# Optimization experiments

Hardware: AMD Instinct MI355X
Metric: run time of the kernel (lower is better)

Reference implementation:

```python
import jax, jax.numpy as jnp
import numpy as np
import math

B, L, D = 4, 4096, 1024
H = 16
DH = D // H  # 64
MAX_SEQ = 8192
NF_MAX = MAX_SEQ // 2 + 1  # 4097
EPS = 1e-6
SQRT2_INV = 1.0 / math.sqrt(2.0)


def _ln(x, scale, bias, eps=1e-5):
    m = jnp.mean(x, axis=-1, keepdims=True)
    v = jnp.mean((x - m) ** 2, axis=-1, keepdims=True)
    return (x - m) * jax.lax.rsqrt(v + eps) * scale + bias


def setup_inputs() -> dict:
    key = jax.random.key(0)
    ks = jax.random.split(key, 16)
    s = 0.02
    inp = {
        'x': jax.random.normal(ks[0], (B, L, D), dtype=jnp.float32),
        'Wq': jax.random.normal(ks[1], (D, D), dtype=jnp.float32) * s,
        'Wv': jax.random.normal(ks[2], (D, D), dtype=jnp.float32) * s,
        'Wo': jax.random.normal(ks[3], (D, D), dtype=jnp.float32) * s,
        # gate MLP: LayerNorm(Dh) -> Linear(Dh,4Dh) -> GELU -> Linear(4Dh, 2*NF_MAX)
        'ln_g_s': jnp.ones((DH,), jnp.float32),
        'ln_g_b': jnp.zeros((DH,), jnp.float32),
        'W1': jax.random.normal(ks[4], (4 * DH, DH), dtype=jnp.float32) * s,
        'b1': jnp.zeros((4 * DH,), jnp.float32),
        'W2': jax.random.normal(ks[5], (2 * NF_MAX, 4 * DH), dtype=jnp.float32) * s,
        'b2': jnp.zeros((2 * NF_MAX,), jnp.float32),
        'modrelu_bias': jnp.zeros((H, NF_MAX), jnp.float32),
        # wavelet gating MLP on head_dim
        'ln_w_s': jnp.ones((DH,), jnp.float32),
        'ln_w_b': jnp.zeros((DH,), jnp.float32),
        'Ww1': jax.random.normal(ks[6], (DH, DH), dtype=jnp.float32) * s,
        'bw1': jnp.zeros((DH,), jnp.float32),
        'Ww2': jax.random.normal(ks[7], (DH, DH), dtype=jnp.float32) * s,
        'bw2': jnp.zeros((DH,), jnp.float32),
    }
    return inp


def _spectre_forward(x, Wq, Wv, Wo, ln_g_s, ln_g_b, W1, b1, W2, b2,
                     modrelu_bias, ln_w_s, ln_w_b, Ww1, bw1, Ww2, bw2):
    b, l, d = x.shape
    n_freq = l // 2 + 1
    # projections -> (B,H,L,Dh)
    q = jnp.einsum('bld,ed->ble', x, Wq).reshape(b, l, H, DH).transpose(0, 2, 1, 3)
    v = jnp.einsum('bld,ed->ble', x, Wv).reshape(b, l, H, DH).transpose(0, 2, 1, 3)
    q_bar = jnp.mean(q, axis=2)  # (B,H,Dh) global query
    # frequency gates from global query
    h = _ln(q_bar, ln_g_s, ln_g_b)
    h = jax.nn.gelu(jnp.einsum('bhd,fd->bhf', h, W1) + b1, approximate=False)
    g = jnp.einsum('bhf,gf->bhg', h, W2) + b2  # (B,H,2*NF_MAX)
    gate = g[..., :n_freq] + 1j * g[..., NF_MAX:NF_MAX + n_freq]  # (B,H,n_freq)
    # spectral mixing along sequence axis
    Vf = jnp.fft.rfft(v, axis=2)  # (B,H,n_freq,Dh) complex
    Vf = Vf * gate[..., None]
    # modReLU nonlinearity on complex spectrum
    mag = jnp.abs(Vf)
    bias = modrelu_bias[None, :, :n_freq, None]
    Vf = Vf * (jax.nn.relu(mag + bias) / (mag + EPS))
    y = jnp.fft.irfft(Vf, n=l, axis=2)  # (B,H,L,Dh)
    # wavelet refinement (eval mode -> never skipped)
    gw = _ln(q_bar, ln_w_s, ln_w_b)
    gw = jax.nn.gelu(jnp.einsum('bhd,ed->bhe', gw, Ww1) + bw1, approximate=False)
    gw = jax.nn.sigmoid(jnp.einsum('bhd,ed->bhe', gw, Ww2) + bw2)  # (B,H,Dh)
    yc = y.transpose(0, 1, 3, 2)  # (B,H,Dh,L)
    low = (yc[..., 0::2] + yc[..., 1::2]) * SQRT2_INV   # Haar analysis LP
    high = (yc[..., 1::2] - yc[..., 0::2]) * SQRT2_INV  # Haar analysis HP
    low = low * gw[..., None]
    high = high * gw[..., None]
    even = (low - high) * SQRT2_INV   # Haar synthesis
    odd = (low + high) * SQRT2_INV
    rec = jnp.stack([even, odd], axis=-1).reshape(b, H, DH, l)  # interleave
    y = y + rec.transpose(0, 1, 3, 2)
    out = jnp.einsum('bld,ed->ble', y.transpose(0, 2, 1, 3).reshape(b, l, d), Wo)
    return out


def reference(x, Wq, Wv, Wo, ln_g_s, ln_g_b, W1, b1, W2, b2,
              modrelu_bias, ln_w_s, ln_w_b, Ww1, bw1, Ww2, bw2):
    return _spectre_forward(x, Wq, Wv, Wo, ln_g_s, ln_g_b, W1, b1, W2, b2,
                            modrelu_bias, ln_w_s, ln_w_b, Ww1, bw1, Ww2, bw2)
```

## Files before the change

### kernel.cpp

```cpp
#include <hip/hip_runtime.h>
#include <math.h>

#define LSEQ 4096
#define DDIM 1024
#define NB 4
#define NH 16
#define DHD 64
#define NFREQ 2049
#define NFMAX 4097

typedef __bf16 bf16_8 __attribute__((ext_vector_type(8)));
typedef float f32x4 __attribute__((ext_vector_type(4)));

__device__ __forceinline__ float gelu_exact(float v) {
    return 0.5f * v * (1.0f + erff(v * 0.70710678118654752440f));
}

__device__ __forceinline__ void gload16(const void* g, void* l) {
    __builtin_amdgcn_global_load_lds((const __attribute__((address_space(1))) char*)g,
                                     (__attribute__((address_space(3))) char*)l, 16, 0, 0);
}

__global__ __launch_bounds__(256) void k_xbar_partial(const float* __restrict__ x, float* __restrict__ xbp,
                                                      __bf16* __restrict__ xbf) {
    int d = blockIdx.x * 256 + threadIdx.x;
    int chunk = blockIdx.y;
    int b = blockIdx.z;
    size_t base = ((size_t)b * LSEQ + (size_t)chunk * 256) * DDIM + d;
    float acc = 0.f;
    for (int l = 0; l < 256; ++l) {
        float v = x[base + (size_t)l * DDIM];
        acc += v;
        xbf[base + (size_t)l * DDIM] = (__bf16)v;
    }
    xbp[(size_t)(b * 16 + chunk) * DDIM + d] = acc;
}

__global__ __launch_bounds__(256) void k_xbar_reduce(const float* __restrict__ xbp, float* __restrict__ xbar) {
    int d = blockIdx.x * 256 + threadIdx.x;
    int b = blockIdx.y;
    float acc = 0.f;
    for (int c = 0; c < 16; ++c) acc += xbp[(size_t)(b * 16 + c) * DDIM + d];
    xbar[b * DDIM + d] = acc * (1.0f / LSEQ);
}

__global__ __launch_bounds__(256) void k_cvt(const float* __restrict__ s, __bf16* __restrict__ d, int n) {
    int i = (blockIdx.x * 256 + threadIdx.x) * 4;
    if (i < n) {
        float4 v = *(const float4*)(s + i);
        d[i] = (__bf16)v.x; d[i + 1] = (__bf16)v.y; d[i + 2] = (__bf16)v.z; d[i + 3] = (__bf16)v.w;
    }
}

__global__ __launch_bounds__(256) void k_qbar(const float* __restrict__ xbar, const float* __restrict__ Wq,
                                              float* __restrict__ qbar) {
    int lane = threadIdx.x & 63;
    int e = blockIdx.x * 4 + (threadIdx.x >> 6);
    const float* wrow = Wq + (size_t)e * DDIM;
    float a0 = 0, a1 = 0, a2 = 0, a3 = 0;
    for (int i = 0; i < 16; ++i) {
        int d = lane + i * 64;
        float w = wrow[d];
        a0 += w * xbar[d];
        a1 += w * xbar[DDIM + d];
        a2 += w * xbar[2 * DDIM + d];
        a3 += w * xbar[3 * DDIM + d];
    }
    for (int off = 32; off > 0; off >>= 1) {
        a0 += __shfl_down(a0, off);
        a1 += __shfl_down(a1, off);
        a2 += __shfl_down(a2, off);
        a3 += __shfl_down(a3, off);
    }
    if (lane == 0) {
        qbar[e] = a0;
        qbar[DDIM + e] = a1;
        qbar[2 * DDIM + e] = a2;
        qbar[3 * DDIM + e] = a3;
    }
}

__global__ __launch_bounds__(256) void k_mlp(const float* __restrict__ qbar,
                                             const float* __restrict__ ln_g_s, const float* __restrict__ ln_g_b,
                                             const float* __restrict__ W1, const float* __restrict__ b1,
                                             const float* __restrict__ ln_w_s, const float* __restrict__ ln_w_b,
                                             const float* __restrict__ Ww1, const float* __restrict__ bw1,
                                             const float* __restrict__ Ww2, const float* __restrict__ bw2,
                                             float* __restrict__ h1g, float* __restrict__ gwp1) {
    int bh = blockIdx.x;
    __shared__ float q[64], hg[64], hw[64], g1[64];
    __shared__ float sm, sv;
    int t = threadIdx.x;
    if (t < 64) q[t] = qbar[bh * 64 + t];
    __syncthreads();
    if (t == 0) {
        float m = 0;
        for (int i = 0; i < 64; ++i) m += q[i];
        m *= (1.0f / 64.0f);
        float v = 0;
        for (int i = 0; i < 64; ++i) { float dd = q[i] - m; v += dd * dd; }
        v *= (1.0f / 64.0f);
        sm = m; sv = v;
    }
    __syncthreads();
    if (t < 64) {
        float n = (q[t] - sm) * rsqrtf(sv + 1e-5f);
        hg[t] = n * ln_g_s[t] + ln_g_b[t];
        hw[t] = n * ln_w_s[t] + ln_w_b[t];
    }
    __syncthreads();
    {
        int f = t;
        const float* w = W1 + (size_t)f * 64;
        float s = b1[f];
        for (int d0 = 0; d0 < 64; ++d0) s += hg[d0] * w[d0];
        h1g[(size_t)bh * 256 + f] = gelu_exact(s);
    }
    if (t < 64) {
        const float* w = Ww1 + (size_t)t * 64;
        float s = bw1[t];
        for (int k = 0; k < 64; ++k) s += hw[k] * w[k];
        g1[t] = gelu_exact(s);
    }
    __syncthreads();
    if (t < 64) {
        const float* w = Ww2 + (size_t)t * 64;
        float s = bw2[t];
        for (int k = 0; k < 64; ++k) s += g1[k] * w[k];
        gwp1[bh * 64 + t] = 1.0f + 1.0f / (1.0f + expf(-s));
    }
}

__global__ __launch_bounds__(256) void k_gate(const float* __restrict__ h1g, const float* __restrict__ W2,
                                              const float* __restrict__ b2,
                                              float* __restrict__ gre, float* __restrict__ gim) {
    int task = blockIdx.x * 4 + (threadIdx.x >> 6);
    if (task >= 2 * NFREQ) return;
    int lane = threadIdx.x & 63;
    int part = task >= NFREQ;
    int f = task - part * NFREQ;
    int row = part ? (NFMAX + f) : f;
    const float* w = W2 + (size_t)row * 256;
    float w0 = w[lane], w1 = w[64 + lane], w2 = w[128 + lane], w3 = w[192 + lane];
    float bias = b2[row];
    float* dst = part ? gim : gre;
    for (int bh = 0; bh < 64; ++bh) {
        const float* hr = h1g + (size_t)bh * 256;
        float p = w0 * hr[lane] + w1 * hr[64 + lane] + w2 * hr[128 + lane] + w3 * hr[192 + lane];
        for (int off = 32; off > 0; off >>= 1) p += __shfl_down(p, off);
        if (lane == 0) dst[(size_t)bh * NFREQ + f] = p + bias;
    }
}

__device__ __forceinline__ void swz256(int bid, int& n0, int& m0, int& b) {
    int w = (bid & 7) * 32 + (bid >> 3);
    b = w >> 6;
    m0 = ((w >> 2) & 15) << 8;
    n0 = (w & 3) << 8;
}

__device__ __forceinline__ void g2_stage(const __bf16* __restrict__ src, int row0, int kt,
                                         __bf16* lds, int tid) {
#pragma unroll
    for (int j = 0; j < 2; ++j) {
        int c = j * 512 + tid;
        int r = c >> 2, kc = (c & 3) * 8;
        __bf16* ldsbase = lds + (size_t)(j * 512 + (tid & ~63)) * 8;
        gload16(src + ((size_t)(row0 + r) << 10) + kt * 32 + kc, ldsbase);
    }
}

__device__ __forceinline__ void g2_core(const __bf16* __restrict__ A, const __bf16* __restrict__ B,
                                        int m0, int n0, __bf16 (*As)[256 * 32], __bf16 (*Bs)[256 * 32],
                                        f32x4 (&acc)[8][4]) {
    int tid = threadIdx.x;
    int lane = tid & 63, w = tid >> 6;
    int wm = w >> 2, wn = w & 3;
    int lrow = lane & 15, lk = (lane >> 4) * 8;
#pragma unroll
    for (int mi = 0; mi < 8; ++mi)
#pragma unroll
        for (int ni = 0; ni < 4; ++ni) acc[mi][ni] = (f32x4){0.f, 0.f, 0.f, 0.f};

    g2_stage(A, m0, 0, As[0], tid);
    g2_stage(B, n0, 0, Bs[0], tid);
    __syncthreads();
    int buf = 0;
    for (int kt = 0; kt < 32; ++kt) {
        if (kt < 31) {
            g2_stage(A, m0, kt + 1, As[buf ^ 1], tid);
            g2_stage(B, n0, kt + 1, Bs[buf ^ 1], tid);
        }
        bf16_8 af[8], bfr[4];
#pragma unroll
        for (int mi = 0; mi < 8; ++mi)
            af[mi] = *(const bf16_8*)&As[buf][(wm * 128 + mi * 16 + lrow) * 32 + lk];
#pragma unroll
        for (int ni = 0; ni < 4; ++ni)
            bfr[ni] = *(const bf16_8*)&Bs[buf][(wn * 64 + ni * 16 + lrow) * 32 + lk];
#pragma unroll
        for (int mi = 0; mi < 8; ++mi)
#pragma unroll
            for (int ni = 0; ni < 4; ++ni)
                acc[mi][ni] = __builtin_amdgcn_mfma_f32_16x16x32_bf16(af[mi], bfr[ni], acc[mi][ni], 0, 0, 0);
        __syncthreads();
        buf ^= 1;
    }
}

__global__ __launch_bounds__(512, 2) void k_vgemm(const __bf16* __restrict__ xbf, const __bf16* __restrict__ Wvb,
                                                  __bf16* __restrict__ vt) {
    __shared__ __align__(16) __bf16 As[2][256 * 32];
    __shared__ __align__(16) __bf16 Bs[2][256 * 32];
    __shared__ __bf16 st[8][16][68];
    int n0, m0, b;
    swz256(blockIdx.x, n0, m0, b);
    f32x4 acc[8][4];
    g2_core(xbf + ((size_t)b << 22), Wvb, m0, n0, As, Bs, acc);
    int tid = threadIdx.x;
    int lane = tid & 63, w = tid >> 6;
    int wm = w >> 2, wn = w & 3;
    size_t vbase = ((size_t)b << 22);
#pragma unroll
    for (int ni = 0; ni < 4; ++ni) {
#pragma unroll
        for (int half = 0; half < 2; ++half) {
#pragma unroll
            for (int ml = 0; ml < 4; ++ml)
#pragma unroll
                for (int r = 0; r < 4; ++r)
                    st[w][lane & 15][ml * 16 + (lane >> 4) * 4 + r] = (__bf16)acc[half * 4 + ml][ni][r];
            asm volatile("" ::: "memory");
#pragma unroll
            for (int er = 0; er < 16; ++er) {
                vt[vbase + (size_t)(n0 + wn * 64 + ni * 16 + er) * LSEQ + m0 + wm * 128 + half * 64 + lane] =
                    st[w][er][lane];
            }
            asm volatile("" ::: "memory");
        }
    }
}

__global__ __launch_bounds__(512, 2) void k_ogemm(const __bf16* __restrict__ ybf, const __bf16* __restrict__ Wob,
                                                  float* __restrict__ out) {
    __shared__ __align__(16) __bf16 As[2][256 * 32];
    __shared__ __align__(16) __bf16 Bs[2][256 * 32];
    int n0, m0, b;
    swz256(blockIdx.x, n0, m0, b);
    f32x4 acc[8][4];
    g2_core(ybf + ((size_t)b << 22), Wob, m0, n0, As, Bs, acc);
    int tid = threadIdx.x;
    int lane = tid & 63, w = tid >> 6;
    int wm = w >> 2, wn = w & 3;
    float* ob = out + ((size_t)b << 22);
#pragma unroll
    for (int mi = 0; mi < 8; ++mi)
#pragma unroll
        for (int ni = 0; ni < 4; ++ni)
#pragma unroll
            for (int r = 0; r < 4; ++r)
                ob[(size_t)(m0 + wm * 128 + mi * 16 + (lane >> 4) * 4 + r) * DDIM +
                   n0 + wn * 64 + ni * 16 + (lane & 15)] = acc[mi][ni][r];
}

__device__ __forceinline__ float2 cmul(float2 a, float2 b) {
    return make_float2(a.x * b.x - a.y * b.y, a.x * b.y + a.y * b.x);
}
__device__ __forceinline__ int P8(int i) { return i + (i >> 3) + (i >> 8); }
__device__ __forceinline__ int SR8(int k) {
    return ((k & 7) << 8) | (((k >> 3) & 7) << 5) | (((k >> 6) & 7) << 2) | (k >> 9);
}

template <int S>
__device__ __forceinline__ void dft4v(float2* x) {
    float2 t0 = make_float2(x[0].x + x[2].x, x[0].y + x[2].y);
    float2 t1 = make_float2(x[0].x - x[2].x, x[0].y - x[2].y);
    float2 t2 = make_float2(x[1].x + x[3].x, x[1].y + x[3].y);
    float2 t3 = make_float2(x[1].x - x[3].x, x[1].y - x[3].y);
    float2 j3 = (S == 1) ? make_float2(t3.y, -t3.x) : make_float2(-t3.y, t3.x);
    x[0] = make_float2(t0.x + t2.x, t0.y + t2.y);
    x[2] = make_float2(t0.x - t2.x, t0.y - t2.y);
    x[1] = make_float2(t1.x + j3.x, t1.y + j3.y);
    x[3] = make_float2(t1.x - j3.x, t1.y - j3.y);
}

template <int S>
__device__ __forceinline__ void dft8v(float2* x) {
    float2 e[4] = {x[0], x[2], x[4], x[6]};
    float2 o[4] = {x[1], x[3], x[5], x[7]};
    dft4v<S>(e);
    dft4v<S>(o);
    const float c = 0.7071067811865476f;
    const float sg = (S == 1) ? -1.f : 1.f;
    o[1] = cmul(o[1], make_float2(c, sg * c));
    o[2] = (S == 1) ? make_float2(o[2].y, -o[2].x) : make_float2(-o[2].y, o[2].x);
    o[3] = cmul(o[3], make_float2(-c, sg * c));
    x[0] = make_float2(e[0].x + o[0].x, e[0].y + o[0].y);
    x[4] = make_float2(e[0].x - o[0].x, e[0].y - o[0].y);
    x[1] = make_float2(e[1].x + o[1].x, e[1].y + o[1].y);
    x[5] = make_float2(e[1].x - o[1].x, e[1].y - o[1].y);
    x[2] = make_float2(e[2].x + o[2].x, e[2].y + o[2].y);
    x[6] = make_float2(e[2].x - o[2].x, e[2].y - o[2].y);
    x[3] = make_float2(e[3].x + o[3].x, e[3].y + o[3].y);
    x[7] = make_float2(e[3].x - o[3].x, e[3].y - o[3].y);
}

template <int S>
__device__ __forceinline__ void tw8(float2* x, int j, float invN) {
    float base = ((S == 1) ? -6.283185307179586f : 6.283185307179586f) * invN;
    float sn, cs;
    __sincosf(base * (float)j, &sn, &cs);
    float2 w1 = make_float2(cs, sn);
    float2 w2 = cmul(w1, w1);
    float2 w3 = cmul(w2, w1);
    float2 w4 = cmul(w2, w2);
    float2 w5 = cmul(w4, w1);
    float2 w6 = cmul(w4, w2);
    float2 w7 = cmul(w4, w3);
    x[1] = cmul(x[1], w1);
    x[2] = cmul(x[2], w2);
    x[3] = cmul(x[3], w3);
    x[4] = cmul(x[4], w4);
    x[5] = cmul(x[5], w5);
    x[6] = cmul(x[6], w6);
    x[7] = cmul(x[7], w7);
}

__global__ __launch_bounds__(256, 2) void k_fft(__bf16* __restrict__ vty,
                                                const float* __restrict__ gre, const float* __restrict__ gim,
                                                const float* __restrict__ mrb, const float* __restrict__ gwp1) {
    __shared__ float2 Zp[2312];
    int pid = blockIdx.x;
    int b = pid >> 10, e = pid & 1023;
    int h = e >> 6, dh = e & 63;
    int bh = b * 16 + h;
    size_t gbase = (size_t)bh * NFREQ;
    size_t mbase = (size_t)h * NFMAX;
    __bf16* row = vty + ((size_t)b << 22) + ((size_t)e << 12);
    int t = threadIdx.x;

#pragma unroll
    for (int cc = 0; cc < 2; ++cc) {
        int c = t + cc * 256;
        bf16_8 a = *(const bf16_8*)&row[c * 8];
#pragma unroll
        for (int q = 0; q < 4; ++q)
            Zp[P8(c * 4 + q)] = make_float2((float)a[2 * q], (float)a[2 * q + 1]);
    }
    __syncthreads();

    float2 x[8];
    {
#pragma unroll
        for (int r = 0; r < 8; ++r) x[r] = Zp[P8(r * 256 + t)];
        dft8v<1>(x);
        tw8<1>(x, t, 1.0f / 2048.0f);
#pragma unroll
        for (int r = 0; r < 8; ++r) Zp[P8(r * 256 + t)] = x[r];
    }
    __syncthreads();
    {
        int g = t >> 5, j = t & 31, base = g * 256 + j;
#pragma unroll
        for (int r = 0; r < 8; ++r) x[r] = Zp[P8(base + r * 32)];
        dft8v<1>(x);
        tw8<1>(x, j, 1.0f / 256.0f);
#pragma unroll
        for (int r = 0; r < 8; ++r) Zp[P8(base + r * 32)] = x[r];
    }
    __syncthreads();
    {
        int g = t >> 2, j = t & 3, base = g * 32 + j;
#pragma unroll
        for (int r = 0; r < 8; ++r) x[r] = Zp[P8(base + r * 4)];
        dft8v<1>(x);
        tw8<1>(x, j, 1.0f / 32.0f);
#pragma unroll
        for (int r = 0; r < 8; ++r) Zp[P8(base + r * 4)] = x[r];
    }
    __syncthreads();
    {
        int base = t * 8;
#pragma unroll
        for (int q = 0; q < 4; ++q) { x[q] = Zp[P8(base + q)]; x[4 + q] = Zp[P8(base + 4 + q)]; }
        dft4v<1>(x);
        dft4v<1>(x + 4);
#pragma unroll
        for (int q = 0; q < 4; ++q) { Zp[P8(base + q)] = x[q]; Zp[P8(base + 4 + q)] = x[4 + q]; }
    }
    __syncthreads();

    {
        float sn0, cs0;
        __sincosf(-1.5339807878856412e-3f * (float)(1 + t), &sn0, &cs0);
        float2 wk = make_float2(cs0, sn0);
        const float2 W256 = make_float2(0.92387953251128675613f, -0.38268343236508977172f);
#pragma unroll
        for (int r = 0; r < 4; ++r) {
            int k = 1 + (r << 8) + t;
            int k2 = 2048 - k;
            int sA = P8(SR8(k)), sB = P8(SR8(k2));
            float cs = wk.x, sn = wk.y;
            float2 Za = Zp[sA], Zb = Zp[sB];
            float Er = 0.5f * (Za.x + Zb.x), Ei = 0.5f * (Za.y - Zb.y);
            float Dr = 0.5f * (Za.x - Zb.x), Di = 0.5f * (Za.y + Zb.y);
            float WDr = cs * Dr - sn * Di, WDi = cs * Di + sn * Dr;
            float Tr = -WDi, Ti = WDr;
            float Vkr = Er - Tr, Vki = Ei - Ti;
            float Vk2r = Er + Tr, Vk2i = -(Ei + Ti);
            float g1r = gre[gbase + k], g1i = gim[gbase + k], b1v = mrb[mbase + k];
            float Ykr = Vkr * g1r - Vki * g1i, Yki = Vkr * g1i + Vki * g1r;
            float m1 = sqrtf(Ykr * Ykr + Yki * Yki);
            float s1 = fmaxf(m1 + b1v, 0.f) / (m1 + 1e-6f);
            Ykr *= s1; Yki *= s1;
            float g2r = gre[gbase + k2], g2i = gim[gbase + k2], b2v = mrb[mbase + k2];
            float Yk2r = Vk2r * g2r - Vk2i * g2i, Yk2i = Vk2r * g2i + Vk2i * g2r;
            float m2 = sqrtf(Yk2r * Yk2r + Yk2i * Yk2i);
            float s2 = fmaxf(m2 + b2v, 0.f) / (m2 + 1e-6f);
            Yk2r *= s2; Yk2i *= s2;
            float Epr = 0.5f * (Ykr + Yk2r), Epi = 0.5f * (Yki - Yk2i);
            float Fr = 0.5f * (Ykr - Yk2r), Fi = 0.5f * (Yki + Yk2i);
            float CWFr = cs * Fr + sn * Fi;
            float CWFi = cs * Fi - sn * Fr;
            Zp[sA] = make_float2(Epr - CWFi, Epi + CWFr);
            Zp[sB] = make_float2(Epr + CWFi, -Epi + CWFr);
            wk = cmul(wk, W256);
        }
    }
    if (t == 0) {
        float2 Z0 = Zp[P8(0)];
        float V0 = Z0.x + Z0.y, VN = Z0.x - Z0.y;
        float g0r = gre[gbase], g0i = gim[gbase], b0v = mrb[mbase];
        float y0r = V0 * g0r, y0i = V0 * g0i;
        float m0 = sqrtf(y0r * y0r + y0i * y0i);
        float Y0 = y0r * (fmaxf(m0 + b0v, 0.f) / (m0 + 1e-6f));
        float gNr = gre[gbase + 2048], gNi = gim[gbase + 2048], bNv = mrb[mbase + 2048];
        float yNr = VN * gNr, yNi = VN * gNi;
        float mN = sqrtf(yNr * yNr + yNi * yNi);
        float YN = yNr * (fmaxf(mN + bNv, 0.f) / (mN + 1e-6f));
        Zp[P8(0)] = make_float2(0.5f * (Y0 + YN), 0.5f * (Y0 - YN));
    }
    __syncthreads();

    {
        int base = t * 8;
#pragma unroll
        for (int q = 0; q < 4; ++q) { x[q] = Zp[P8(base + q)]; x[4 + q] = Zp[P8(base + 4 + q)]; }
        dft4v<-1>(x);
        dft4v<-1>(x + 4);
#pragma unroll
        for (int q = 0; q < 4; ++q) { Zp[P8(base + q)] = x[q]; Zp[P8(base + 4 + q)] = x[4 + q]; }
    }
    __syncthreads();
    {
        int g = t >> 2, j = t & 3, base = g * 32 + j;
#pragma unroll
        for (int r = 0; r < 8; ++r) x[r] = Zp[P8(base + r * 4)];
        tw8<-1>(x, j, 1.0f / 32.0f);
        dft8v<-1>(x);
#pragma unroll
        for (int r = 0; r < 8; ++r) Zp[P8(base + r * 4)] = x[r];
    }
    __syncthreads();
    {
        int g = t >> 5, j = t & 31, base = g * 256 + j;
#pragma unroll
        for (int r = 0; r < 8; ++r) x[r] = Zp[P8(base + r * 32)];
        tw8<-1>(x, j, 1.0f / 256.0f);
        dft8v<-1>(x);
#pragma unroll
        for (int r = 0; r < 8; ++r) Zp[P8(base + r * 32)] = x[r];
    }
    __syncthreads();
    {
#pragma unroll
        for (int r = 0; r < 8; ++r) x[r] = Zp[P8(r * 256 + t)];
        tw8<-1>(x, t, 1.0f / 2048.0f);
        dft8v<-1>(x);
        float sc = gwp1[bh * 64 + dh] * (1.0f / 2048.0f);
        unsigned int* row32 = (unsigned int*)row;
#pragma unroll
        for (int r = 0; r < 8; ++r) {
            __bf16 h1 = (__bf16)(x[r].x * sc);
            __bf16 h2 = (__bf16)(x[r].y * sc);
            unsigned int u = (unsigned int)__builtin_bit_cast(unsigned short, h1) |
                             ((unsigned int)__builtin_bit_cast(unsigned short, h2) << 16);
            row32[t + 256 * r] = u;
        }
    }
}

__global__ __launch_bounds__(256) void k_t2(const __bf16* __restrict__ vt, __bf16* __restrict__ ybf) {
    __shared__ __bf16 tl[64][66];
    int e0 = blockIdx.x * 64, l0 = blockIdx.y * 64, b = blockIdx.z;
    int t = threadIdx.x;
    const __bf16* src = vt + ((size_t)b << 22);
    __bf16* dst = ybf + ((size_t)b << 22);
    int er = t >> 3, lc = (t & 7) * 8;
#pragma unroll
    for (int it = 0; it < 2; ++it) {
        int e = er + it * 32;
        bf16_8 v = *(const bf16_8*)&src[(size_t)(e0 + e) * LSEQ + l0 + lc];
#pragma unroll
        for (int j = 0; j < 8; ++j) tl[e][lc + j] = v[j];
    }
    __syncthreads();
    int lr = t >> 3, ec = (t & 7) * 8;
#pragma unroll
    for (int it = 0; it < 2; ++it) {
        int l = lr + it * 32;
        bf16_8 v;
#pragma unroll
        for (int j = 0; j < 8; ++j) v[j] = tl[ec + j][l];
        *(bf16_8*)&dst[(size_t)(l0 + l) * DDIM + e0 + ec] = v;
    }
}

extern "C" void kernel_launch(void* const* d_in, const int* in_sizes, int n_in,
                              void* d_out, int out_size, void* d_ws, size_t ws_size,
                              hipStream_t stream) {
    const float* x      = (const float*)d_in[0];
    const float* Wq     = (const float*)d_in[1];
    const float* Wv     = (const float*)d_in[2];
    const float* Wo     = (const float*)d_in[3];
    const float* ln_g_s = (const float*)d_in[4];
    const float* ln_g_b = (const float*)d_in[5];
    const float* W1     = (const float*)d_in[6];
    const float* b1     = (const float*)d_in[7];
    const float* W2     = (const float*)d_in[8];
    const float* b2     = (const float*)d_in[9];
    const float* mrb    = (const float*)d_in[10];
    const float* ln_w_s = (const float*)d_in[11];
    const float* ln_w_b = (const float*)d_in[12];
    const float* Ww1    = (const float*)d_in[13];
    const float* bw1    = (const float*)d_in[14];
    const float* Ww2    = (const float*)d_in[15];
    const float* bw2    = (const float*)d_in[16];
    float* out = (float*)d_out;

    char* W = (char*)d_ws;
    __bf16* xbf = (__bf16*)W;
    __bf16* ybf = xbf;
    __bf16* Wvb = (__bf16*)(W + 33554432);
    __bf16* Wob = (__bf16*)(W + 35651584);
    float*  xbp = (float*)(W + 37748736);
    float*  xbar= (float*)(W + 38010880);
    float*  qbar= (float*)(W + 38027264);
    float*  h1g = (float*)(W + 38043648);
    float*  gwp1= (float*)(W + 38109184);
    float*  gre = (float*)(W + 38125568);
    float*  gim = (float*)(W + 38650112);

    __bf16* vt = (__bf16*)d_out;

    k_xbar_partial<<<dim3(4, 16, 4), 256, 0, stream>>>(x, xbp, xbf);
    k_cvt<<<1024, 256, 0, stream>>>(Wv, Wvb, DDIM * DDIM);
    k_cvt<<<1024, 256, 0, stream>>>(Wo, Wob, DDIM * DDIM);
    k_xbar_reduce<<<dim3(4, 4), 256, 0, stream>>>(xbp, xbar);
    k_qbar<<<256, 256, 0, stream>>>(xbar, Wq, qbar);
    k_mlp<<<64, 256, 0, stream>>>(qbar, ln_g_s, ln_g_b, W1, b1, ln_w_s, ln_w_b,
                                  Ww1, bw1, Ww2, bw2, h1g, gwp1);
    k_gate<<<1025, 256, 0, stream>>>(h1g, W2, b2, gre, gim);
    k_vgemm<<<256, 512, 0, stream>>>(xbf, Wvb, vt);
    k_fft<<<4096, 256, 0, stream>>>(vt, gre, gim, mrb, gwp1);
    k_t2<<<dim3(16, 64, 4), 256, 0, stream>>>(vt, ybf);
    k_ogemm<<<256, 512, 0, stream>>>(ybf, Wob, out);
}
```

Baseline: 224.7 us.

## Restructure bf16 GEMM core with 64-wide K tiles, XOR-swizzled LDS and deeper prefetch

The shared GEMM core used by the V and output projections now stages 64-wide K tiles instead of 32-wide, halving the number of loop iterations and barriers. Loads go into an XOR-swizzled LDS layout so MFMA fragment reads avoid bank conflicts. Prefetch runs two stages ahead, with explicit vmcnt/lgkmcnt waits and raw barriers in place of __syncthreads, and s_setprio raises priority around the MFMA bursts. The cost is a much larger LDS footprint (about 128 KB, plus a staging buffer in the V GEMM), which likely limits each CU to one block despite launch_bounds(512,2).

```diff
diff --git a/kernel.cpp b/kernel.cpp
--- a/kernel.cpp
+++ b/kernel.cpp
@@ -159,64 +159,97 @@
     n0 = (w & 3) << 8;
 }
 
-__device__ __forceinline__ void g2_stage(const __bf16* __restrict__ src, int row0, int kt,
-                                         __bf16* lds, int tid) {
+__device__ __forceinline__ void g3_stage_half(const __bf16* __restrict__ src, int row0, int kt,
+                                              char* ldshalf, int tid) {
 #pragma unroll
     for (int j = 0; j < 2; ++j) {
         int c = j * 512 + tid;
-        int r = c >> 2, kc = (c & 3) * 8;
-        __bf16* ldsbase = lds + (size_t)(j * 512 + (tid & ~63)) * 8;
-        gload16(src + ((size_t)(row0 + r) << 10) + kt * 32 + kc, ldsbase);
-    }
-}
-
-__device__ __forceinline__ void g2_core(const __bf16* __restrict__ A, const __bf16* __restrict__ B,
-                                        int m0, int n0, __bf16 (*As)[256 * 32], __bf16 (*Bs)[256 * 32],
-                                        f32x4 (&acc)[8][4]) {
+        int r = c >> 3;
+        int kc = ((c & 7) ^ (r & 7)) * 8;
+        char* dst = ldshalf + (size_t)(j * 512 + (tid & ~63)) * 16;
+        gload16(src + ((size_t)(row0 + r) << 10) + kt * 64 + kc, dst);
+    }
+}
+
+__device__ __forceinline__ void g3_compute(const char* L, int db, int wm, int wn,
+                                           int lrow, int lsl, f32x4 (&acc)[8][4]) {
+    const char* Ab = L + db * 32768 + wm * 16384;
+    const char* Bb = L + 65536 + db * 32768 + (wn >> 1) * 16384;
+    int xs = lrow & 7;
+    int brb = (wn & 1) * 64;
+#pragma unroll
+    for (int kk = 0; kk < 2; ++kk) {
+        int slot = ((kk * 4 + lsl) ^ xs) << 4;
+        bf16_8 af[8], bfr[4];
+#pragma unroll
+        for (int mi = 0; mi < 8; ++mi)
+            af[mi] = *(const bf16_8*)(Ab + (mi * 16 + lrow) * 128 + slot);
+#pragma unroll
+        for (int ni = 0; ni < 4; ++ni)
+            bfr[ni] = *(const bf16_8*)(Bb + (brb + ni * 16 + lrow) * 128 + slot);
+        __builtin_amdgcn_s_setprio(1);
+#pragma unroll
+        for (int mi = 0; mi < 8; ++mi)
+#pragma unroll
+            for (int ni = 0; ni < 4; ++ni)
+                acc[mi][ni] = __builtin_amdgcn_mfma_f32_16x16x32_bf16(af[mi], bfr[ni], acc[mi][ni], 0, 0, 0);
+        __builtin_amdgcn_s_setprio(0);
+    }
+}
+
+__device__ __forceinline__ void g3_core(const __bf16* __restrict__ A, const __bf16* __restrict__ B,
+                                        int m0, int n0, char* L, f32x4 (&acc)[8][4]) {
     int tid = threadIdx.x;
     int lane = tid & 63, w = tid >> 6;
     int wm = w >> 2, wn = w & 3;
-    int lrow = lane & 15, lk = (lane >> 4) * 8;
+    int lrow = lane & 15, lsl = lane >> 4;
 #pragma unroll
     for (int mi = 0; mi < 8; ++mi)
 #pragma unroll
         for (int ni = 0; ni < 4; ++ni) acc[mi][ni] = (f32x4){0.f, 0.f, 0.f, 0.f};
 
-    g2_stage(A, m0, 0, As[0], tid);
-    g2_stage(B, n0, 0, Bs[0], tid);
-    __syncthreads();
-    int buf = 0;
-    for (int kt = 0; kt < 32; ++kt) {
-        if (kt < 31) {
-            g2_stage(A, m0, kt + 1, As[buf ^ 1], tid);
-            g2_stage(B, n0, kt + 1, Bs[buf ^ 1], tid);
+#define G3_STAGE(KT, DB)                                                        \
+    do {                                                                        \
+        g3_stage_half(A, m0,       (KT), L + (DB) * 32768,               tid);  \
+        g3_stage_half(A, m0 + 128, (KT), L + (DB) * 32768 + 16384,       tid);  \
+        g3_stage_half(B, n0,       (KT), L + 65536 + (DB) * 32768,       tid);  \
+        g3_stage_half(B, n0 + 128, (KT), L + 65536 + (DB) * 32768 + 16384, tid);\
+    } while (0)
+
+    G3_STAGE(0, 0);
+    G3_STAGE(1, 1);
+    asm volatile("s_waitcnt vmcnt(8)" ::: "memory");
+    __builtin_amdgcn_s_barrier();
+    asm volatile("" ::: "memory");
+#pragma unroll 1
+    for (int kt = 0; kt < 16; ++kt) {
+        int db = kt & 1;
+        g3_compute(L, db, wm, wn, lrow, lsl, acc);
+        asm volatile("s_waitcnt lgkmcnt(0)" ::: "memory");
+        __builtin_amdgcn_s_barrier();
+        asm volatile("" ::: "memory");
+        if (kt < 14) {
+            G3_STAGE(kt + 2, db);
+            asm volatile("s_waitcnt vmcnt(8)" ::: "memory");
+            __builtin_amdgcn_s_barrier();
+            asm volatile("" ::: "memory");
+        } else if (kt == 14) {
+            asm volatile("s_waitcnt vmcnt(0)" ::: "memory");
+            __builtin_amdgcn_s_barrier();
+            asm volatile("" ::: "memory");
         }
-        bf16_8 af[8], bfr[4];
-#pragma unroll
-        for (int mi = 0; mi < 8; ++mi)
-            af[mi] = *(const bf16_8*)&As[buf][(wm * 128 + mi * 16 + lrow) * 32 + lk];
-#pragma unroll
-        for (int ni = 0; ni < 4; ++ni)
-            bfr[ni] = *(const bf16_8*)&Bs[buf][(wn * 64 + ni * 16 + lrow) * 32 + lk];
-#pragma unroll
-        for (int mi = 0; mi < 8; ++mi)
-#pragma unroll
-            for (int ni = 0; ni < 4; ++ni)
-                acc[mi][ni] = __builtin_amdgcn_mfma_f32_16x16x32_bf16(af[mi], bfr[ni], acc[mi][ni], 0, 0, 0);
-        __syncthreads();
-        buf ^= 1;
-    }
+    }
+#undef G3_STAGE
 }
 
 __global__ __launch_bounds__(512, 2) void k_vgemm(const __bf16* __restrict__ xbf, const __bf16* __restrict__ Wvb,
                                                   __bf16* __restrict__ vt) {
-    __shared__ __align__(16) __bf16 As[2][256 * 32];
-    __shared__ __align__(16) __bf16 Bs[2][256 * 32];
-    __shared__ __bf16 st[8][16][68];
+    __shared__ __align__(16) char L[131072 + 17408];
+    __bf16 (*st)[16][68] = (__bf16(*)[16][68])(L + 131072);
     int n0, m0, b;
     swz256(blockIdx.x, n0, m0, b);
     f32x4 acc[8][4];
-    g2_core(xbf + ((size_t)b << 22), Wvb, m0, n0, As, Bs, acc);
+    g3_core(xbf + ((size_t)b << 22), Wvb, m0, n0, L, acc);
     int tid = threadIdx.x;
     int lane = tid & 63, w = tid >> 6;
     int wm = w >> 2, wn = w & 3;
@@ -243,12 +276,11 @@
 
 __global__ __launch_bounds__(512, 2) void k_ogemm(const __bf16* __restrict__ ybf, const __bf16* __restrict__ Wob,
                                                   float* __restrict__ out) {
-    __shared__ __align__(16) __bf16 As[2][256 * 32];
-    __shared__ __align__(16) __bf16 Bs[2][256 * 32];
+    __shared__ __align__(16) char L[131072];
     int n0, m0, b;
     swz256(blockIdx.x, n0, m0, b);
     f32x4 acc[8][4];
-    g2_core(ybf + ((size_t)b << 22), Wob, m0, n0, As, Bs, acc);
+    g3_core(ybf + ((size_t)b << 22), Wob, m0, n0, L, acc);
     int tid = threadIdx.x;
     int lane = tid & 63, w = tid >> 6;
     int wm = w >> 2, wn = w & 3;
```

Result: faster. 201.0 us (-10.5%).
